# Kernel tuning notes

Hardware: AMD Instinct MI355X
Metric: run time of the kernel (lower is better)

The kernel has to match this reference:

```python
import jax, jax.numpy as jnp
import numpy as np


def setup_inputs() -> dict:
    B, M, N, DEG, MAX_ITER = 256, 8192, 16384, 10, 30
    key = jax.random.key(0)
    k1, k2 = jax.random.split(key)
    rng = np.random.default_rng(0)
    cols = rng.integers(0, N, size=(M, DEG))
    cols[::2, -1] = N  # dummy (padding) entries on half the check rows; index N is the dummy column
    V_c_col = jnp.asarray(cols, dtype=jnp.int32)
    V_c_row = jnp.asarray(np.repeat(np.arange(M)[:, None], DEG, axis=1), dtype=jnp.int32)
    synd = jax.random.randint(k1, (B, M), 0, 2).astype(jnp.float32)
    llr0 = jax.random.normal(k2, (B, N), dtype=jnp.float32) + 2.0  # LLRs biased toward 'no error'
    return {"synd": synd, "llr0": llr0, "V_c_row": V_c_row, "V_c_col": V_c_col, "max_iter": MAX_ITER}


def _decode(synd, llr0, V_c_row, V_c_col, max_iter):
    B, M = synd.shape
    N = llr0.shape[1]
    dtype = llr0.dtype
    mask_dummy = (V_c_col == N)            # [M, DEG]
    cols_flat = V_c_col.reshape(-1)        # [M*DEG]
    inf = jnp.asarray(jnp.inf, dtype)
    # extended variable axis: real variables + one dummy column pinned to +inf LLR
    u_init = jnp.concatenate([llr0, jnp.full((B, 1), jnp.inf, dtype)], axis=1)   # [B, N+1]
    synd_neg = jnp.where(synd == 0, 1.0, -1.0).astype(dtype)[:, V_c_row]          # [B, M, DEG]
    message0 = u_init[:, V_c_col]                                                 # [B, M, DEG]
    l_v0 = jnp.zeros((B, N + 1), dtype)
    zeros_bn = jnp.zeros((B, N + 1), dtype)
    init = (message0, l_v0, zeros_bn, zeros_bn,
            jnp.full((B,), -1, jnp.int32), jnp.zeros((B,), jnp.int32))

    def step(carry, i):
        message, l_v, e_out, l_out, num_iters, conv = carry
        # vn_update: first iteration passes initial messages through unchanged
        a = jnp.where(i == 1, message, l_v[:, V_c_col] - message)
        # cn_update: normalized min-sum, beta = 1 - 2^{-i}
        beta = jnp.asarray(1.0, dtype) - jnp.power(jnp.asarray(2.0, dtype), -(i.astype(dtype)))
        sign = jnp.sign(a)
        sign = jnp.where(sign == 0, jnp.asarray(-1.0, dtype), sign)
        q_sign = synd_neg * jnp.prod(sign, axis=2, keepdims=True)
        ab = jnp.abs(a)
        srt = jnp.sort(ab, axis=2)
        min0, min1 = srt[:, :, :1], srt[:, :, 1:2]
        min_res = jnp.where(ab == min0, min1, min0)
        b = beta * sign * q_sign * min_res
        b = jnp.where(mask_dummy[None, :, :], jnp.asarray(0.0, dtype), b)
        # llr_update: scatter-add check->variable messages onto the intrinsic LLRs
        l_v = u_init.at[:, cols_flat].add(b.reshape(B, -1))
        l_v = l_v.at[:, -1].set(inf)
        e_v = (l_v <= 0).astype(dtype)
        # syndrome estimation: parity of the estimated error over each check's support
        s_est = jnp.mod(jnp.sum(e_v[:, V_c_col], axis=2), 2.0).astype(dtype)
        ok = jnp.all(s_est == synd, axis=1) & (num_iters == -1)
        num_iters = jnp.where(ok, i.astype(jnp.int32), num_iters)
        conv = jnp.where(ok, 1, conv)
        e_out = jnp.where(ok[:, None], e_v, e_out)
        l_out = jnp.where(ok[:, None], l_v, l_out)
        return (b, l_v, e_out, l_out, num_iters, conv), None

    (message, l_v, e_out, l_out, num_iters, conv), _ = jax.lax.scan(
        step, init, jnp.arange(1, max_iter + 1))
    # rows that never converged take the final-iteration estimate
    unconv = num_iters == -1
    e_v = (l_v <= 0).astype(dtype)
    e_out = jnp.where(unconv[:, None], e_v, e_out)
    l_out = jnp.where(unconv[:, None], l_v, l_out)
    num_iters = jnp.where(unconv, max_iter, num_iters)
    # drop the dummy column, matching e_out[:, :-1] / l_out[:, :-1]
    return e_out[:, :-1], num_iters, l_out[:, :-1], conv


def reference(synd, llr0, V_c_row, V_c_col, max_iter):
    return _decode(synd, llr0, V_c_row, V_c_col, max_iter)
```

## Files before the change

### kernel.cpp

```cpp
#include <hip/hip_runtime.h>
#include <cmath>
#include <cstdint>
#include <cstddef>

#define BB 256
#define MM 8192
#define NN 16384
#define DEG 10
#define MAX_ITER 30
#define PAR_BLOCKS 64

typedef unsigned char  u8;
typedef unsigned short u16;


__global__ void k_init(int* colcnt, int* colfill, int* mm, int* niter, int* conv, int* cnt) {
    int t = blockIdx.x * blockDim.x + threadIdx.x;
    if (t < NN) { colcnt[t] = 0; colfill[t] = 0; }
    if (t < BB) { mm[t] = 0; niter[t] = -1; conv[t] = 0; }
    if (t == 0) *cnt = 0;
}

__global__ void k_transpose_f32(const float* __restrict__ in, float* __restrict__ out,
                                float* __restrict__ out2, int R, int C) {
    __shared__ float tile[64][65];
    int c0 = blockIdx.x * 64;
    int r0 = blockIdx.y * 64;
    #pragma unroll
    for (int k = 0; k < 16; k++) {
        int idx = k * 256 + threadIdx.x;
        int i = idx >> 6, j = idx & 63;
        tile[i][j] = in[(size_t)(r0 + i) * C + (c0 + j)];
    }
    __syncthreads();
    #pragma unroll
    for (int k = 0; k < 16; k++) {
        int idx = k * 256 + threadIdx.x;
        int i = idx >> 6, j = idx & 63;
        float v = tile[j][i];
        size_t o = (size_t)(c0 + i) * R + (r0 + j);
        out[o] = v;
        if (out2) out2[o] = v;
    }
}

__global__ void k_synd_t(const float* __restrict__ synd, u8* __restrict__ syndb) {
    __shared__ float tile[64][65];
    int c0 = blockIdx.x * 64;
    int r0 = blockIdx.y * 64;
    #pragma unroll
    for (int k = 0; k < 16; k++) {
        int idx = k * 256 + threadIdx.x;
        int i = idx >> 6, j = idx & 63;
        tile[i][j] = synd[(size_t)(r0 + i) * MM + (c0 + j)];
    }
    __syncthreads();
    #pragma unroll
    for (int k = 0; k < 16; k++) {
        int idx = k * 256 + threadIdx.x;
        int i = idx >> 6, j = idx & 63;
        syndb[(size_t)(c0 + i) * BB + (r0 + j)] = (tile[j][i] != 0.0f) ? 1 : 0;
    }
}

__global__ void k_hist(const int* __restrict__ vc, int* colcnt) {
    int e = blockIdx.x * 256 + threadIdx.x;
    if (e >= MM * DEG) return;
    int c = vc[e];
    if (c < NN) atomicAdd(&colcnt[c], 1);
}

__global__ void k_scan(const int* __restrict__ colcnt, int* __restrict__ colptr) {
    __shared__ int part[256];
    __shared__ int base[257];
    int t = threadIdx.x;
    int s = 0;
    for (int i = 0; i < 64; i++) s += colcnt[t * 64 + i];
    part[t] = s;
    __syncthreads();
    if (t == 0) {
        int acc = 0;
        for (int i = 0; i < 256; i++) { base[i] = acc; acc += part[i]; }
        base[256] = acc;
    }
    __syncthreads();
    int acc = base[t];
    for (int i = 0; i < 64; i++) { int c = t * 64 + i; colptr[c] = acc; acc += colcnt[c]; }
    if (t == 255) colptr[NN] = base[256];
}

__global__ void k_fill(const int* __restrict__ vc, const int* __restrict__ colptr,
                       int* colfill, int* coledges) {
    int e = blockIdx.x * 256 + threadIdx.x;
    if (e >= MM * DEG) return;
    int c = vc[e];
    if (c < NN) {
        int p = colptr[c] + atomicAdd(&colfill[c], 1);
        coledges[p] = e;
    }
}

__global__ void k_sort(const int* __restrict__ colptr, int* coledges) {
    int n = blockIdx.x * 256 + threadIdx.x;
    if (n >= NN) return;
    int p0 = colptr[n], p1 = colptr[n + 1];
    for (int i = p0 + 1; i < p1; i++) {
        int v = coledges[i];
        int j = i - 1;
        while (j >= p0 && coledges[j] > v) { coledges[j + 1] = coledges[j]; j--; }
        coledges[j + 1] = v;
    }
}


__global__ void k_check(const int* __restrict__ vc, const float* __restrict__ lv,
                        float* __restrict__ sv0, float* __restrict__ sv1,
                        u16* __restrict__ sbits, const u8* __restrict__ syndb,
                        float beta, int first) {
    __shared__ int cs[DEG];
    int m = blockIdx.x, t = threadIdx.x;
    if (t < DEG) cs[t] = vc[m * DEG + t];
    __syncthreads();
    int b2 = t * 2;
    size_t mb = (size_t)m * BB + b2;

    float pv0x = 0.f, pv0y = 0.f, pv1x = 0.f, pv1y = 0.f;
    unsigned pbx = 0, pby = 0;
    if (!first) {
        float2 a0 = *(const float2*)(sv0 + mb);
        float2 a1 = *(const float2*)(sv1 + mb);
        ushort2 pb = *(const ushort2*)(sbits + mb);
        pv0x = a0.x; pv0y = a0.y; pv1x = a1.x; pv1y = a1.y;
        pbx = pb.x; pby = pb.y;
    }
    int pi0x = (pbx >> 11) & 15, pi0y = (pby >> 11) & 15;
    unsigned pqx = (pbx >> 10) & 1u, pqy = (pby >> 10) & 1u;

    float m0x = INFINITY, m1x = INFINITY, m0y = INFINITY, m1y = INFINITY;
    unsigned negx = 0, negy = 0;
    int i0x = 0, i0y = 0;

    #pragma unroll
    for (int d = 0; d < DEG; d++) {
        int c = cs[d];
        float ax, ay;
        if (c >= NN) {
            ax = INFINITY; ay = INFINITY;
        } else {
            float2 g = *(const float2*)(lv + (size_t)c * BB + b2);
            if (first) { ax = g.x; ay = g.y; }
            else {
                float tx = (d == pi0x) ? pv1x : pv0x;
                float ty = (d == pi0y) ? pv1y : pv0y;
                unsigned sx = pqx ^ ((pbx >> d) & 1u);
                unsigned sy = pqy ^ ((pby >> d) & 1u);
                ax = g.x - (sx ? -tx : tx);
                ay = g.y - (sy ? -ty : ty);
            }
        }
        if (!(ax > 0.0f)) negx |= 1u << d;
        if (!(ay > 0.0f)) negy |= 1u << d;
        float xx = fabsf(ax), xy = fabsf(ay);
        if (xx < m0x) { m1x = m0x; m0x = xx; i0x = d; } else if (xx < m1x) m1x = xx;
        if (xy < m0y) { m1y = m0y; m0y = xy; i0y = d; } else if (xy < m1y) m1y = xy;
    }
    uchar2 sb = *(const uchar2*)(syndb + mb);
    unsigned qx = (__popc(negx) & 1u) ^ (sb.x ? 1u : 0u);
    unsigned qy = (__popc(negy) & 1u) ^ (sb.y ? 1u : 0u);

    *(float2*)(sv0 + mb) = make_float2(beta * m0x, beta * m0y);
    *(float2*)(sv1 + mb) = make_float2(beta * m1x, beta * m1y);
    ushort2 nb;
    nb.x = (u16)(negx | (qx << 10) | ((unsigned)i0x << 11));
    nb.y = (u16)(negy | (qy << 10) | ((unsigned)i0y << 11));
    *(ushort2*)(sbits + mb) = nb;
}

__global__ void k_var(const float* __restrict__ llr0t,
                      const float* __restrict__ sv0, const float* __restrict__ sv1,
                      const u16* __restrict__ sbits,
                      const int* __restrict__ colptr, const int* __restrict__ coledges,
                      float* __restrict__ lv, const int* __restrict__ niter) {
    int n = blockIdx.x, t = threadIdx.x, b2 = t * 2;
    int f0 = niter[b2], f1 = niter[b2 + 1];
    if (f0 != -1 && f1 != -1) return;
    float2 s = *(const float2*)(llr0t + (size_t)n * BB + b2);
    int p0 = colptr[n], p1 = colptr[n + 1];
    for (int p = p0; p < p1; p++) {
        int e = coledges[p];
        int m = (int)(((long long)e * 0x66666667LL) >> 34);
        int d = e - m * DEG;
        size_t mb = (size_t)m * BB + b2;
        float2 v0 = *(const float2*)(sv0 + mb);
        float2 v1 = *(const float2*)(sv1 + mb);
        ushort2 bb = *(const ushort2*)(sbits + mb);
        float tx = (d == ((bb.x >> 11) & 15)) ? v1.x : v0.x;
        float ty = (d == ((bb.y >> 11) & 15)) ? v1.y : v0.y;
        unsigned sx = ((bb.x >> 10) ^ (bb.x >> d)) & 1u;
        unsigned sy = ((bb.y >> 10) ^ (bb.y >> d)) & 1u;
        s.x += sx ? -tx : tx;
        s.y += sy ? -ty : ty;
    }
    float* dst = lv + (size_t)n * BB + b2;
    if (f0 == -1 && f1 == -1) *(float2*)dst = s;
    else if (f0 == -1) dst[0] = s.x;
    else dst[1] = s.y;
}

__global__ void k_parity(const int* __restrict__ vc, const float* __restrict__ lv,
                         const u8* __restrict__ syndb, int* __restrict__ niter,
                         int* __restrict__ conv, int* __restrict__ mm,
                         int* __restrict__ cnt, int it) {
    __shared__ int s_stop, s_last;
    int b = threadIdx.x;
    bool frozen = (niter[b] != -1);
    volatile int* vmm = (volatile int*)mm;

    for (int m = blockIdx.x; m < MM; m += PAR_BLOCKS) {
        if (b == 0) s_stop = 1;
        __syncthreads();
        bool flagged = frozen || (vmm[b] != 0);
        if (!flagged) s_stop = 0;
        __syncthreads();
        if (s_stop) break;
        if (!flagged) {
            unsigned par = 0;
            #pragma unroll
            for (int d = 0; d < DEG; d++) {
                int c = vc[m * DEG + d];
                if (c < NN) par ^= (lv[(size_t)c * BB + b] <= 0.0f) ? 1u : 0u;
            }
            if (par != (unsigned)syndb[(size_t)m * BB + b]) atomicOr(&mm[b], 1);
        }
    }
    __syncthreads();
    __threadfence();
    if (b == 0) {
        int tk = atomicAdd(cnt, 1);
        s_last = (tk == PAR_BLOCKS - 1) ? 1 : 0;
    }
    __syncthreads();
    if (s_last) {
        __threadfence();
        if (niter[b] == -1 && mm[b] == 0) { niter[b] = it; conv[b] = 1; }
        mm[b] = 0;
        if (b == 0) *cnt = 0;
    }
}


__global__ void k_out_e(const float* __restrict__ lv, float* __restrict__ out) {
    __shared__ float tile[64][65];
    int c0 = blockIdx.x * 64;
    int r0 = blockIdx.y * 64;
    #pragma unroll
    for (int k = 0; k < 16; k++) {
        int idx = k * 256 + threadIdx.x;
        int i = idx >> 6, j = idx & 63;
        tile[i][j] = (lv[(size_t)(r0 + i) * BB + (c0 + j)] <= 0.0f) ? 1.0f : 0.0f;
    }
    __syncthreads();
    #pragma unroll
    for (int k = 0; k < 16; k++) {
        int idx = k * 256 + threadIdx.x;
        int i = idx >> 6, j = idx & 63;
        out[(size_t)(c0 + i) * NN + (r0 + j)] = tile[j][i];
    }
}

__global__ void k_out_scalars(const int* __restrict__ niter, const int* __restrict__ conv,
                              float* __restrict__ out_ni, float* __restrict__ out_conv) {
    int b = threadIdx.x;
    int ni = niter[b];
    out_ni[b] = (float)(ni == -1 ? MAX_ITER : ni);
    out_conv[b] = (float)conv[b];
}


extern "C" void kernel_launch(void* const* d_in, const int* in_sizes, int n_in,
                              void* d_out, int out_size, void* d_ws, size_t ws_size,
                              hipStream_t stream) {
    const float* synd = (const float*)d_in[0];
    const float* llr0 = (const float*)d_in[1];
    const int* vcol   = (const int*)d_in[3];
    float* out = (float*)d_out;

    char* ws = (char*)d_ws;
    size_t off = 0;
    auto alloc = [&](size_t bytes) {
        off = (off + 255) & ~(size_t)255;
        size_t o = off; off += bytes; return o;
    };
    float* llr0t  = (float*)(ws + alloc((size_t)NN * BB * 4));
    float* lv     = (float*)(ws + alloc((size_t)NN * BB * 4));
    float* sv0    = (float*)(ws + alloc((size_t)MM * BB * 4));
    float* sv1    = (float*)(ws + alloc((size_t)MM * BB * 4));
    u16*   sbits  = (u16*)(ws + alloc((size_t)MM * BB * 2));
    u8*   syndb   = (u8*)(ws + alloc((size_t)MM * BB));
    int* coledges = (int*)(ws + alloc((size_t)MM * DEG * 4));
    int* colptr   = (int*)(ws + alloc((size_t)(NN + 1) * 4));
    int* colcnt   = (int*)(ws + alloc((size_t)NN * 4));
    int* colfill  = (int*)(ws + alloc((size_t)NN * 4));
    int* mm       = (int*)(ws + alloc((size_t)BB * 4));
    int* niter    = (int*)(ws + alloc((size_t)BB * 4));
    int* conv     = (int*)(ws + alloc((size_t)BB * 4));
    int* cnt      = (int*)(ws + alloc(256));
    (void)in_sizes; (void)n_in; (void)out_size; (void)ws_size;

    k_init<<<NN / 256, 256, 0, stream>>>(colcnt, colfill, mm, niter, conv, cnt);
    k_transpose_f32<<<dim3(NN / 64, BB / 64), 256, 0, stream>>>(llr0, llr0t, lv, BB, NN);
    k_synd_t<<<dim3(MM / 64, BB / 64), 256, 0, stream>>>(synd, syndb);
    k_hist<<<(MM * DEG + 255) / 256, 256, 0, stream>>>(vcol, colcnt);
    k_scan<<<1, 256, 0, stream>>>(colcnt, colptr);
    k_fill<<<(MM * DEG + 255) / 256, 256, 0, stream>>>(vcol, colptr, colfill, coledges);
    k_sort<<<NN / 256, 256, 0, stream>>>(colptr, coledges);

    for (int i = 1; i <= MAX_ITER; i++) {
        float beta = 1.0f - ldexpf(1.0f, -i);
        k_check<<<MM, 128, 0, stream>>>(vcol, lv, sv0, sv1, sbits, syndb,
                                        beta, (i == 1) ? 1 : 0);
        k_var<<<NN, 128, 0, stream>>>(llr0t, sv0, sv1, sbits, colptr, coledges, lv, niter);
        k_parity<<<PAR_BLOCKS, 256, 0, stream>>>(vcol, lv, syndb, niter, conv, mm, cnt, i);
    }

    size_t off_e = 0;
    size_t off_ni = (size_t)BB * NN;
    size_t off_l = off_ni + BB;
    size_t off_c = off_l + (size_t)BB * NN;
    k_out_e<<<dim3(BB / 64, NN / 64), 256, 0, stream>>>(lv, out + off_e);
    k_transpose_f32<<<dim3(BB / 64, NN / 64), 256, 0, stream>>>(lv, out + off_l, nullptr, NN, BB);
    k_out_scalars<<<1, 256, 0, stream>>>(niter, conv, out + off_ni, out + off_c);
}
```

Measured before the change: 2.031 ms.

## Widen per-thread batch to four lanes, interleave check messages, fuse parity into check

Check and variable kernels now handle four batch lanes per thread with float4 loads and pack four rows or columns per 256-thread block. The separate min0 and min1 buffers are interleaved into one buffer, so one row's messages come in two wide loads. The previous iteration's parity/convergence check now runs inside the first 64 blocks of the next check kernel, with one final standalone parity launch after the loop. This is meant to cut memory transactions and kernel launches per iteration. In exchange it adds register pressure and coarser early-exit granularity in the variable kernel, which only returns when all four lanes have converged.

Result: slower. 2.094 ms (+3.1%).

```diff
diff --git a/kernel.cpp b/kernel.cpp
--- a/kernel.cpp
+++ b/kernel.cpp
@@ -113,98 +113,176 @@
 }
 
 
-__global__ void k_check(const int* __restrict__ vc, const float* __restrict__ lv,
-                        float* __restrict__ sv0, float* __restrict__ sv1,
-                        u16* __restrict__ sbits, const u8* __restrict__ syndb,
-                        float beta, int first) {
-    __shared__ int cs[DEG];
-    int m = blockIdx.x, t = threadIdx.x;
-    if (t < DEG) cs[t] = vc[m * DEG + t];
-    __syncthreads();
-    int b2 = t * 2;
-    size_t mb = (size_t)m * BB + b2;
-
-    float pv0x = 0.f, pv0y = 0.f, pv1x = 0.f, pv1y = 0.f;
-    unsigned pbx = 0, pby = 0;
+__global__ void k_check4(const int* __restrict__ vc, const float* __restrict__ lv,
+                         float* __restrict__ svv, u16* __restrict__ sbits,
+                         const u8* __restrict__ syndb,
+                         int* __restrict__ niter, int* __restrict__ conv,
+                         int* __restrict__ mm, int* __restrict__ cnt,
+                         float beta, int first, int it_prev) {
+    __shared__ int cs[4 * DEG];
+    __shared__ int s_stop, s_last;
+    int bid = blockIdx.x, t = threadIdx.x;
+
+    if (it_prev > 0 && bid < PAR_BLOCKS) {
+        bool frozen = (niter[t] != -1);
+        volatile int* vmm = (volatile int*)mm;
+        for (int m = bid; m < MM; m += PAR_BLOCKS) {
+            if (t == 0) s_stop = 1;
+            __syncthreads();
+            bool flagged = frozen || (vmm[t] != 0);
+            if (!flagged) s_stop = 0;
+            __syncthreads();
+            if (s_stop) break;
+            if (!flagged) {
+                unsigned par = 0;
+                #pragma unroll
+                for (int d = 0; d < DEG; d++) {
+                    int c = vc[m * DEG + d];
+                    if (c < NN) par ^= (lv[(size_t)c * BB + t] <= 0.0f) ? 1u : 0u;
+                }
+                if (par != (unsigned)syndb[(size_t)m * BB + t]) atomicOr(&mm[t], 1);
+            }
+        }
+        __syncthreads();
+        __threadfence();
+        if (t == 0) {
+            int tk = atomicAdd(cnt, 1);
+            s_last = (tk == PAR_BLOCKS - 1) ? 1 : 0;
+        }
+        __syncthreads();
+        if (s_last) {
+            int mmv = atomicAdd(&mm[t], 0);
+            if (niter[t] == -1 && mmv == 0) { niter[t] = it_prev; conv[t] = 1; }
+            mm[t] = 0;
+            if (t == 0) *cnt = 0;
+            __threadfence();
+        }
+        __syncthreads();
+    }
+
+    if (t < 4 * DEG) cs[t] = vc[bid * 4 * DEG + t];
+    __syncthreads();
+
+    int w = t >> 6, l = t & 63;
+    int m = bid * 4 + w, b4 = l * 4;
+    size_t mb = (size_t)m * BB + b4;
+
+    float pv0[4], pv1[4];
+    unsigned pb[4];
     if (!first) {
-        float2 a0 = *(const float2*)(sv0 + mb);
-        float2 a1 = *(const float2*)(sv1 + mb);
-        ushort2 pb = *(const ushort2*)(sbits + mb);
-        pv0x = a0.x; pv0y = a0.y; pv1x = a1.x; pv1y = a1.y;
-        pbx = pb.x; pby = pb.y;
-    }
-    int pi0x = (pbx >> 11) & 15, pi0y = (pby >> 11) & 15;
-    unsigned pqx = (pbx >> 10) & 1u, pqy = (pby >> 10) & 1u;
-
-    float m0x = INFINITY, m1x = INFINITY, m0y = INFINITY, m1y = INFINITY;
-    unsigned negx = 0, negy = 0;
-    int i0x = 0, i0y = 0;
+        float4 q0 = *(const float4*)(svv + mb * 2);
+        float4 q1 = *(const float4*)(svv + mb * 2 + 4);
+        ushort4 pbv = *(const ushort4*)(sbits + mb);
+        pv0[0] = q0.x; pv1[0] = q0.y; pv0[1] = q0.z; pv1[1] = q0.w;
+        pv0[2] = q1.x; pv1[2] = q1.y; pv0[3] = q1.z; pv1[3] = q1.w;
+        pb[0] = pbv.x; pb[1] = pbv.y; pb[2] = pbv.z; pb[3] = pbv.w;
+    } else {
+        #pragma unroll
+        for (int j = 0; j < 4; j++) { pv0[j] = 0.f; pv1[j] = 0.f; pb[j] = 0; }
+    }
+    int pi0[4]; unsigned pq[4];
+    #pragma unroll
+    for (int j = 0; j < 4; j++) { pi0[j] = (pb[j] >> 11) & 15; pq[j] = (pb[j] >> 10) & 1u; }
+
+    float m0[4] = {INFINITY, INFINITY, INFINITY, INFINITY};
+    float m1[4] = {INFINITY, INFINITY, INFINITY, INFINITY};
+    unsigned neg[4] = {0, 0, 0, 0};
+    int i0[4] = {0, 0, 0, 0};
 
     #pragma unroll
     for (int d = 0; d < DEG; d++) {
-        int c = cs[d];
-        float ax, ay;
-        if (c >= NN) {
-            ax = INFINITY; ay = INFINITY;
-        } else {
-            float2 g = *(const float2*)(lv + (size_t)c * BB + b2);
-            if (first) { ax = g.x; ay = g.y; }
+        int c = cs[w * DEG + d];
+        if (c >= NN) continue;
+        float4 g = *(const float4*)(lv + (size_t)c * BB + b4);
+        float gj[4] = {g.x, g.y, g.z, g.w};
+        #pragma unroll
+        for (int j = 0; j < 4; j++) {
+            float a;
+            if (first) a = gj[j];
             else {
-                float tx = (d == pi0x) ? pv1x : pv0x;
-                float ty = (d == pi0y) ? pv1y : pv0y;
-                unsigned sx = pqx ^ ((pbx >> d) & 1u);
-                unsigned sy = pqy ^ ((pby >> d) & 1u);
-                ax = g.x - (sx ? -tx : tx);
-                ay = g.y - (sy ? -ty : ty);
+                float tt = (d == pi0[j]) ? pv1[j] : pv0[j];
+                unsigned sx = pq[j] ^ ((pb[j] >> d) & 1u);
+                a = gj[j] - (sx ? -tt : tt);
             }
-        }
-        if (!(ax > 0.0f)) negx |= 1u << d;
-        if (!(ay > 0.0f)) negy |= 1u << d;
-        float xx = fabsf(ax), xy = fabsf(ay);
-        if (xx < m0x) { m1x = m0x; m0x = xx; i0x = d; } else if (xx < m1x) m1x = xx;
-        if (xy < m0y) { m1y = m0y; m0y = xy; i0y = d; } else if (xy < m1y) m1y = xy;
-    }
-    uchar2 sb = *(const uchar2*)(syndb + mb);
-    unsigned qx = (__popc(negx) & 1u) ^ (sb.x ? 1u : 0u);
-    unsigned qy = (__popc(negy) & 1u) ^ (sb.y ? 1u : 0u);
-
-    *(float2*)(sv0 + mb) = make_float2(beta * m0x, beta * m0y);
-    *(float2*)(sv1 + mb) = make_float2(beta * m1x, beta * m1y);
-    ushort2 nb;
-    nb.x = (u16)(negx | (qx << 10) | ((unsigned)i0x << 11));
-    nb.y = (u16)(negy | (qy << 10) | ((unsigned)i0y << 11));
-    *(ushort2*)(sbits + mb) = nb;
-}
-
-__global__ void k_var(const float* __restrict__ llr0t,
-                      const float* __restrict__ sv0, const float* __restrict__ sv1,
-                      const u16* __restrict__ sbits,
-                      const int* __restrict__ colptr, const int* __restrict__ coledges,
-                      float* __restrict__ lv, const int* __restrict__ niter) {
-    int n = blockIdx.x, t = threadIdx.x, b2 = t * 2;
-    int f0 = niter[b2], f1 = niter[b2 + 1];
-    if (f0 != -1 && f1 != -1) return;
-    float2 s = *(const float2*)(llr0t + (size_t)n * BB + b2);
+            if (!(a > 0.0f)) neg[j] |= 1u << d;
+            float x = fabsf(a);
+            if (x < m0[j]) { m1[j] = m0[j]; m0[j] = x; i0[j] = d; }
+            else if (x < m1[j]) m1[j] = x;
+        }
+    }
+
+    uchar4 sb = *(const uchar4*)(syndb + mb);
+    unsigned sbv[4] = {sb.x, sb.y, sb.z, sb.w};
+    unsigned q[4];
+    #pragma unroll
+    for (int j = 0; j < 4; j++)
+        q[j] = (__popc(neg[j]) & 1u) ^ (sbv[j] ? 1u : 0u);
+
+    float v0[4], v1[4];
+    #pragma unroll
+    for (int j = 0; j < 4; j++) { v0[j] = beta * m0[j]; v1[j] = beta * m1[j]; }
+
+    *(float4*)(svv + mb * 2)     = make_float4(v0[0], v1[0], v0[1], v1[1]);
+    *(float4*)(svv + mb * 2 + 4) = make_float4(v0[2], v1[2], v0[3], v1[3]);
+    ushort4 nb;
+    nb.x = (u16)(neg[0] | (q[0] << 10) | ((unsigned)i0[0] << 11));
+    nb.y = (u16)(neg[1] | (q[1] << 10) | ((unsigned)i0[1] << 11));
+    nb.z = (u16)(neg[2] | (q[2] << 10) | ((unsigned)i0[2] << 11));
+    nb.w = (u16)(neg[3] | (q[3] << 10) | ((unsigned)i0[3] << 11));
+    *(ushort4*)(sbits + mb) = nb;
+}
+
+__global__ void k_var4(const float* __restrict__ llr0t, const float* __restrict__ svv,
+                       const u16* __restrict__ sbits,
+                       const int* __restrict__ colptr, const int* __restrict__ coledges,
+                       float* __restrict__ lv, const int* __restrict__ niter) {
+    int t = threadIdx.x;
+    int w = t >> 6, l = t & 63;
+    int n = blockIdx.x * 4 + w, b4 = l * 4;
+
+    int4 f = *(const int4*)(niter + b4);
+    if (f.x != -1 && f.y != -1 && f.z != -1 && f.w != -1) return;
+
+    float4 s = *(const float4*)(llr0t + (size_t)n * BB + b4);
     int p0 = colptr[n], p1 = colptr[n + 1];
-    for (int p = p0; p < p1; p++) {
-        int e = coledges[p];
-        int m = (int)(((long long)e * 0x66666667LL) >> 34);
+    for (int pp = p0; pp < p1; pp++) {
+        int e = coledges[pp];
+        int m = e / DEG;
         int d = e - m * DEG;
-        size_t mb = (size_t)m * BB + b2;
-        float2 v0 = *(const float2*)(sv0 + mb);
-        float2 v1 = *(const float2*)(sv1 + mb);
-        ushort2 bb = *(const ushort2*)(sbits + mb);
-        float tx = (d == ((bb.x >> 11) & 15)) ? v1.x : v0.x;
-        float ty = (d == ((bb.y >> 11) & 15)) ? v1.y : v0.y;
-        unsigned sx = ((bb.x >> 10) ^ (bb.x >> d)) & 1u;
-        unsigned sy = ((bb.y >> 10) ^ (bb.y >> d)) & 1u;
-        s.x += sx ? -tx : tx;
-        s.y += sy ? -ty : ty;
-    }
-    float* dst = lv + (size_t)n * BB + b2;
-    if (f0 == -1 && f1 == -1) *(float2*)dst = s;
-    else if (f0 == -1) dst[0] = s.x;
-    else dst[1] = s.y;
+        size_t mb = (size_t)m * BB + b4;
+        float4 q0 = *(const float4*)(svv + mb * 2);
+        float4 q1 = *(const float4*)(svv + mb * 2 + 4);
+        ushort4 bb = *(const ushort4*)(sbits + mb);
+        {
+            float tt = (d == ((bb.x >> 11) & 15)) ? q0.y : q0.x;
+            unsigned sx = ((bb.x >> 10) ^ (bb.x >> d)) & 1u;
+            s.x += sx ? -tt : tt;
+        }
+        {
+            float tt = (d == ((bb.y >> 11) & 15)) ? q0.w : q0.z;
+            unsigned sx = ((bb.y >> 10) ^ (bb.y >> d)) & 1u;
+            s.y += sx ? -tt : tt;
+        }
+        {
+            float tt = (d == ((bb.z >> 11) & 15)) ? q1.y : q1.x;
+            unsigned sx = ((bb.z >> 10) ^ (bb.z >> d)) & 1u;
+            s.z += sx ? -tt : tt;
+        }
+        {
+            float tt = (d == ((bb.w >> 11) & 15)) ? q1.w : q1.z;
+            unsigned sx = ((bb.w >> 10) ^ (bb.w >> d)) & 1u;
+            s.w += sx ? -tt : tt;
+        }
+    }
+    float* dst = lv + (size_t)n * BB + b4;
+    if (f.x == -1 && f.y == -1 && f.z == -1 && f.w == -1) {
+        *(float4*)dst = s;
+    } else {
+        if (f.x == -1) dst[0] = s.x;
+        if (f.y == -1) dst[1] = s.y;
+        if (f.z == -1) dst[2] = s.z;
+        if (f.w == -1) dst[3] = s.w;
+    }
 }
 
 __global__ void k_parity(const int* __restrict__ vc, const float* __restrict__ lv,
@@ -241,8 +319,8 @@
     }
     __syncthreads();
     if (s_last) {
-        __threadfence();
-        if (niter[b] == -1 && mm[b] == 0) { niter[b] = it; conv[b] = 1; }
+        int mmv = atomicAdd(&mm[b], 0);
+        if (niter[b] == -1 && mmv == 0) { niter[b] = it; conv[b] = 1; }
         mm[b] = 0;
         if (b == 0) *cnt = 0;
     }
@@ -293,8 +371,7 @@
     };
     float* llr0t  = (float*)(ws + alloc((size_t)NN * BB * 4));
     float* lv     = (float*)(ws + alloc((size_t)NN * BB * 4));
-    float* sv0    = (float*)(ws + alloc((size_t)MM * BB * 4));
-    float* sv1    = (float*)(ws + alloc((size_t)MM * BB * 4));
+    float* svv    = (float*)(ws + alloc((size_t)MM * BB * 8));
     u16*   sbits  = (u16*)(ws + alloc((size_t)MM * BB * 2));
     u8*   syndb   = (u8*)(ws + alloc((size_t)MM * BB));
     int* coledges = (int*)(ws + alloc((size_t)MM * DEG * 4));
@@ -317,17 +394,18 @@
 
     for (int i = 1; i <= MAX_ITER; i++) {
         float beta = 1.0f - ldexpf(1.0f, -i);
-        k_check<<<MM, 128, 0, stream>>>(vcol, lv, sv0, sv1, sbits, syndb,
-                                        beta, (i == 1) ? 1 : 0);
-        k_var<<<NN, 128, 0, stream>>>(llr0t, sv0, sv1, sbits, colptr, coledges, lv, niter);
-        k_parity<<<PAR_BLOCKS, 256, 0, stream>>>(vcol, lv, syndb, niter, conv, mm, cnt, i);
-    }
-
-    size_t off_e = 0;
-    size_t off_ni = (size_t)BB * NN;
-    size_t off_l = off_ni + BB;
-    size_t off_c = off_l + (size_t)BB * NN;
-    k_out_e<<<dim3(BB / 64, NN / 64), 256, 0, stream>>>(lv, out + off_e);
-    k_transpose_f32<<<dim3(BB / 64, NN / 64), 256, 0, stream>>>(lv, out + off_l, nullptr, NN, BB);
-    k_out_scalars<<<1, 256, 0, stream>>>(niter, conv, out + off_ni, out + off_c);
-}
+        k_check4<<<MM / 4, 256, 0, stream>>>(vcol, lv, svv, sbits, syndb,
+                                             niter, conv, mm, cnt,
+                                             beta, (i == 1) ? 1 : 0, i - 1);
+        k_var4<<<NN / 4, 256, 0, stream>>>(llr0t, svv, sbits, colptr, coledges, lv, niter);
+    }
+    k_parity<<<PAR_BLOCKS, 256, 0, stream>>>(vcol, lv, syndb, niter, conv, mm, cnt, MAX_ITER);
+
+    float* out_e    = out;
+    float* out_ni   = out + (size_t)BB * NN;
+    float* out_l    = out + (size_t)BB * NN + BB;
+    float* out_conv = out + 2 * (size_t)BB * NN + BB;
+    k_out_e<<<dim3(BB / 64, NN / 64), 256, 0, stream>>>(lv, out_e);
+    k_transpose_f32<<<dim3(BB / 64, NN / 64), 256, 0, stream>>>(lv, out_l, nullptr, NN, BB);
+    k_out_scalars<<<1, 256, 0, stream>>>(niter, conv, out_ni, out_conv);
+}
```
